# Kernel optimization log

Hardware: AMD Instinct MI355X
Metric: run time of the kernel (lower is better)

## Reference

```python
import jax, jax.numpy as jnp
import numpy as np

N_QUBITS = 8
DIM = 2 ** N_QUBITS  # 256
N_CYCLES = 4
BATCH = 8192

# ---- gate matrices (work for scalar or batched [B] angles) ----

def _rz(t):
    e0 = jnp.exp(-0.5j * t.astype(jnp.complex64))
    e1 = jnp.exp(0.5j * t.astype(jnp.complex64))
    z = jnp.zeros_like(e0)
    return jnp.stack([jnp.stack([e0, z], -1), jnp.stack([z, e1], -1)], -2)


def _ry(t):
    c = jnp.cos(t / 2)
    s = jnp.sin(t / 2)
    m = jnp.stack([jnp.stack([c, -s], -1), jnp.stack([s, c], -1)], -2)
    return m.astype(jnp.complex64)


def _u3(t, p, l):
    ct = jnp.cos(t / 2).astype(jnp.complex64)
    st = jnp.sin(t / 2).astype(jnp.complex64)
    ep = jnp.exp(1j * p.astype(jnp.complex64))
    el = jnp.exp(1j * l.astype(jnp.complex64))
    return jnp.stack([jnp.stack([ct, -el * st], -1),
                      jnp.stack([ep * st, ep * el * ct], -1)], -2)

# ---- state-vector gate application (wire 0 = most significant, torchquantum convention) ----

def apply_1q(psi, U, w):
    B = psi.shape[0]
    p = psi.reshape(B, 2 ** w, 2, -1)
    if U.ndim == 3:
        p = jnp.einsum('bij,bajc->baic', U, p)
    else:
        p = jnp.einsum('ij,bajc->baic', U, p)
    return p.reshape(B, DIM)


def apply_cnot(psi, c, t):
    p = psi.reshape((-1,) + (2,) * N_QUBITS)
    c_ax, t_ax = c + 1, t + 1
    p0 = jax.lax.index_in_dim(p, 0, c_ax, keepdims=True)
    p1 = jnp.flip(jax.lax.index_in_dim(p, 1, c_ax, keepdims=True), axis=t_ax)
    return jnp.concatenate([p0, p1], axis=c_ax).reshape(-1, DIM)


def expval_z(psi, w):
    pr = (psi.real ** 2 + psi.imag ** 2).reshape(psi.shape[0], 2 ** w, 2, -1)
    pr = pr.sum(axis=(1, 3))
    return pr[:, 0] - pr[:, 1]


def conv_block(psi, hi, lo, rza, rzb, rzc, rya, ryb):
    # rz(hi); cnot(hi,lo); rz(lo); ry(hi); cnot(lo,hi); ry(hi); cnot(hi,lo); rz(lo)
    psi = apply_1q(psi, _rz(rza), hi)
    psi = apply_cnot(psi, hi, lo)
    psi = apply_1q(psi, _rz(rzb), lo)
    psi = apply_1q(psi, _ry(rya), hi)
    psi = apply_cnot(psi, lo, hi)
    psi = apply_1q(psi, _ry(ryb), hi)
    psi = apply_cnot(psi, hi, lo)
    psi = apply_1q(psi, _rz(rzc), lo)
    return psi


def _forward(theta, phi, rz_angles, ry_angles, u3_params, w1, b1, w2, b2):
    B = theta.shape[0]
    psi = jnp.zeros((B, DIM), jnp.complex64).at[:, 0].set(1.0)
    # circuit builder (assumed): per cycle RY(theta), RZ(phi) on every wire + CNOT ring
    Ury = _ry(theta)  # [B,2,2]
    Urz = _rz(phi)
    for _ in range(N_CYCLES):
        for w in range(N_QUBITS):
            psi = apply_1q(psi, Ury, w)
        for w in range(N_QUBITS):
            psi = apply_1q(psi, Urz, w)
        for w in range(N_QUBITS):
            psi = apply_cnot(psi, w, (w + 1) % N_QUBITS)
    # conv layer 1: pairs (1,0),(3,2),(5,4),(7,6) using rz1-12, ry1-8
    for i, (hi, lo) in enumerate([(1, 0), (3, 2), (5, 4), (7, 6)]):
        psi = conv_block(psi, hi, lo, rz_angles[3 * i], rz_angles[3 * i + 1],
                         rz_angles[3 * i + 2], ry_angles[2 * i], ry_angles[2 * i + 1])
    # intermediate expvals on [0,2,4,6] are computed-and-discarded in the original (non-collapsing): no-op
    for j, w in enumerate([1, 3, 5, 7]):
        psi = apply_1q(psi, _u3(u3_params[j, 0], u3_params[j, 1], u3_params[j, 2]), w)
    # conv layer 2: pairs (3,1),(7,5),(5,3) using rz13-21, ry9-14
    for k, (hi, lo) in enumerate([(3, 1), (7, 5), (5, 3)]):
        i = 4 + k
        psi = conv_block(psi, hi, lo, rz_angles[3 * i], rz_angles[3 * i + 1],
                         rz_angles[3 * i + 2], ry_angles[2 * i], ry_angles[2 * i + 1])
    # discarded expvals on [1,5]: no-op
    psi = apply_1q(psi, _u3(u3_params[4, 0], u3_params[4, 1], u3_params[4, 2]), 3)
    psi = apply_1q(psi, _u3(u3_params[5, 0], u3_params[5, 1], u3_params[5, 2]), 7)
    x = jnp.stack([expval_z(psi, 3), expval_z(psi, 7)], axis=-1)  # [B,2] real
    h = jnp.tanh(x @ w1.T + b1)
    y = h @ w2.T + b2
    return jax.nn.sigmoid(y)  # [B,1]


def setup_inputs() -> dict:
    key = jax.random.key(0)
    ks = jax.random.split(key, 9)
    return {
        'theta': jax.random.normal(ks[0], (BATCH,), jnp.float32),
        'phi': jax.random.normal(ks[1], (BATCH,), jnp.float32),
        'rz_angles': jax.random.normal(ks[2], (21,), jnp.float32),
        'ry_angles': jax.random.normal(ks[3], (14,), jnp.float32),
        'u3_params': jax.random.normal(ks[4], (6, 3), jnp.float32),
        'w1': jax.random.normal(ks[5], (10, 2), jnp.float32) * 0.5,
        'b1': jax.random.normal(ks[6], (10,), jnp.float32) * 0.1,
        'w2': jax.random.normal(ks[7], (1, 10), jnp.float32) * 0.3,
        'b2': jax.random.normal(ks[8], (1,), jnp.float32) * 0.1,
    }


def reference(theta, phi, rz_angles, ry_angles, u3_params, w1, b1, w2, b2):
    return _forward(theta, phi, rz_angles, ry_angles, u3_params, w1, b1, w2, b2)
```

## Files before the change

kernel.cpp:

```cpp
#include <hip/hip_runtime.h>
#include <math.h>


constexpr int NREG = 8;

typedef float v2f __attribute__((ext_vector_type(2)));

__device__ __forceinline__ v2f vfma(v2f a, v2f b, v2f c) {
  return __builtin_elementwise_fma(a, b, c);
}
__device__ __forceinline__ v2f splat(float x) { return (v2f){x, x}; }

template<int MASK>
__device__ __forceinline__ float lxor(float x) {
  int xi = __float_as_int(x);
  int r;
  if constexpr (MASK == 1)      r = __builtin_amdgcn_mov_dpp(xi, 0xB1, 0xF, 0xF, true);
  else if constexpr (MASK == 2) r = __builtin_amdgcn_mov_dpp(xi, 0x4E, 0xF, 0xF, true);
  else                          r = __builtin_amdgcn_ds_swizzle(xi, (MASK << 10) | 0x1F);
  return __int_as_float(r);
}

template<int MASK>
__device__ __forceinline__ v2f lxor2(v2f v) {
  v2f r;
  r.x = lxor<MASK>(v.x);
  r.y = lxor<MASK>(v.y);
  return r;
}

struct State {
  v2f a[NREG];
};


template<int P>
__device__ __forceinline__ void ry_gate(State& st, float c, float s, int L) {
  if constexpr (P <= 2) {
    constexpr int m = 1 << P;
    #pragma unroll
    for (int r0 = 0; r0 < NREG; ++r0) {
      if (r0 & m) continue;
      const int r1 = r0 | m;
      v2f a0 = st.a[r0], a1 = st.a[r1];
      st.a[r0] = vfma(splat(-s), a1, splat(c) * a0);
      st.a[r1] = vfma(splat( s), a0, splat(c) * a1);
    }
  } else {
    constexpr int m = 1 << (P - 3);
    float ss = ((L >> (P - 3)) & 1) ? s : -s;
    #pragma unroll
    for (int r = 0; r < NREG; ++r) {
      v2f b = lxor2<m>(st.a[r]);
      st.a[r] = vfma(splat(ss), b, splat(c) * st.a[r]);
    }
  }
}

template<int P>
__device__ __forceinline__ void rz_gate(State& st, float cz, float sz, int L) {
  if constexpr (P <= 2) {
    #pragma unroll
    for (int r = 0; r < NREG; ++r) {
      float sg = ((r >> P) & 1) ? sz : -sz;
      v2f v = st.a[r];
      st.a[r] = vfma((v2f){-sg, sg}, v.yx, splat(cz) * v);
    }
  } else {
    float sg = ((L >> (P - 3)) & 1) ? sz : -sz;
    #pragma unroll
    for (int r = 0; r < NREG; ++r) {
      v2f v = st.a[r];
      st.a[r] = vfma((v2f){-sg, sg}, v.yx, splat(cz) * v);
    }
  }
}

template<int PC, int PT>
__device__ __forceinline__ void cnot_gate(State& st, int L) {
  if constexpr (PT <= 2) {
    constexpr int mt = 1 << PT;
    if constexpr (PC <= 2) {
      constexpr int mc = 1 << PC;
      #pragma unroll
      for (int r0 = 0; r0 < NREG; ++r0) {
        if (!(r0 & mc) || (r0 & mt)) continue;
        const int r1 = r0 | mt;
        v2f t = st.a[r0]; st.a[r0] = st.a[r1]; st.a[r1] = t;
      }
    } else {
      bool cb = (L >> (PC - 3)) & 1;
      #pragma unroll
      for (int r0 = 0; r0 < NREG; ++r0) {
        if (r0 & mt) continue;
        const int r1 = r0 | mt;
        v2f a0 = st.a[r0], a1 = st.a[r1];
        st.a[r0] = cb ? a1 : a0;
        st.a[r1] = cb ? a0 : a1;
      }
    }
  } else {
    constexpr int mt = 1 << (PT - 3);
    if constexpr (PC <= 2) {
      constexpr int mc = 1 << PC;
      #pragma unroll
      for (int r = 0; r < NREG; ++r) {
        if (!(r & mc)) continue;
        st.a[r] = lxor2<mt>(st.a[r]);
      }
    } else {
      bool cb = (L >> (PC - 3)) & 1;
      #pragma unroll
      for (int r = 0; r < NREG; ++r) {
        v2f b = lxor2<mt>(st.a[r]);
        st.a[r] = cb ? b : st.a[r];
      }
    }
  }
}

__device__ __forceinline__ v2f cmac(v2f t, v2f u, v2f v) {
  t = vfma(splat(u.x), v, t);
  t = vfma((v2f){-u.y, u.y}, v.yx, t);
  return t;
}

__device__ __forceinline__ v2f ld2(const float* p) {
  return (v2f){p[0], p[1]};
}


template<int MH, int ML>
__device__ __forceinline__ void apply_G_ll(State& st, const float* g, int L) {
  const int bh = (L & MH) ? 1 : 0;
  const int bl = (L & ML) ? 1 : 0;
  const int row = (bh << 1) | bl;
  const float* gr = g + row * 8;
  const v2f cS = ld2(gr + 2 * row);
  const v2f cL = ld2(gr + 2 * (row ^ 1));
  const v2f cH = ld2(gr + 2 * (row ^ 2));
  const v2f cB = ld2(gr + 2 * (row ^ 3));
  #pragma unroll
  for (int r = 0; r < NREG; ++r) {
    v2f v = st.a[r];
    v2f pl = lxor2<ML>(v);
    v2f ph = lxor2<MH>(v);
    v2f pb = lxor2<MH | ML>(v);
    v2f t = (v2f){0.f, 0.f};
    t = cmac(t, cS, v);
    t = cmac(t, cL, pl);
    t = cmac(t, cH, ph);
    t = cmac(t, cB, pb);
    st.a[r] = t;
  }
}

template<int MHR, int MLR>
__device__ __forceinline__ void apply_G_rr(State& st, const float* g) {
  #pragma unroll
  for (int base = 0; base < NREG; ++base) {
    if (base & (MHR | MLR)) continue;
    v2f in0 = st.a[base];
    v2f in1 = st.a[base | MLR];
    v2f in2 = st.a[base | MHR];
    v2f in3 = st.a[base | MHR | MLR];
    #pragma unroll
    for (int i = 0; i < 4; ++i) {
      v2f t = (v2f){0.f, 0.f};
      t = cmac(t, ld2(g + i * 8 + 0), in0);
      t = cmac(t, ld2(g + i * 8 + 2), in1);
      t = cmac(t, ld2(g + i * 8 + 4), in2);
      t = cmac(t, ld2(g + i * 8 + 6), in3);
      if (i == 0) st.a[base] = t;
      else if (i == 1) st.a[base | MLR] = t;
      else if (i == 2) st.a[base | MHR] = t;
      else st.a[base | MHR | MLR] = t;
    }
  }
}

template<int MREG, int ML>
__device__ __forceinline__ void apply_G_mx(State& st, const float* g, int L) {
  const int bl = (L & ML) ? 1 : 0;
  const int r0w = bl;
  const int r1w = 2 + bl;
  const float* g0 = g + r0w * 8;
  const float* g1 = g + r1w * 8;
  const v2f c0S = ld2(g0 + 2 * r0w),       c0L = ld2(g0 + 2 * (r0w ^ 1));
  const v2f c0H = ld2(g0 + 2 * (r0w ^ 2)), c0B = ld2(g0 + 2 * (r0w ^ 3));
  const v2f c1S = ld2(g1 + 2 * r1w),       c1L = ld2(g1 + 2 * (r1w ^ 1));
  const v2f c1H = ld2(g1 + 2 * (r1w ^ 2)), c1B = ld2(g1 + 2 * (r1w ^ 3));
  v2f x[NREG];
  #pragma unroll
  for (int r = 0; r < NREG; ++r) x[r] = lxor2<ML>(st.a[r]);
  v2f o[NREG];
  #pragma unroll
  for (int r = 0; r < NREG; ++r) {
    v2f t = (v2f){0.f, 0.f};
    if (r & MREG) {
      t = cmac(t, c1S, st.a[r]);
      t = cmac(t, c1L, x[r]);
      t = cmac(t, c1H, st.a[r ^ MREG]);
      t = cmac(t, c1B, x[r ^ MREG]);
    } else {
      t = cmac(t, c0S, st.a[r]);
      t = cmac(t, c0L, x[r]);
      t = cmac(t, c0H, st.a[r ^ MREG]);
      t = cmac(t, c0B, x[r ^ MREG]);
    }
    o[r] = t;
  }
  #pragma unroll
  for (int r = 0; r < NREG; ++r) st.a[r] = o[r];
}


__device__ __forceinline__ void b_phase(float* cr, float* ci, int i, float pc, float ps) {
  float r = cr[i] * pc - ci[i] * ps;
  float m = cr[i] * ps + ci[i] * pc;
  cr[i] = r; ci[i] = m;
}
__device__ __forceinline__ void b_rz_hi(float* cr, float* ci, float t) {
  float s, c; sincosf(0.5f * t, &s, &c);
  b_phase(cr, ci, 0, c, -s); b_phase(cr, ci, 1, c, -s);
  b_phase(cr, ci, 2, c,  s); b_phase(cr, ci, 3, c,  s);
}
__device__ __forceinline__ void b_rz_lo(float* cr, float* ci, float t) {
  float s, c; sincosf(0.5f * t, &s, &c);
  b_phase(cr, ci, 0, c, -s); b_phase(cr, ci, 2, c, -s);
  b_phase(cr, ci, 1, c,  s); b_phase(cr, ci, 3, c,  s);
}
__device__ __forceinline__ void b_ry_hi(float* cr, float* ci, float t) {
  float s, c; sincosf(0.5f * t, &s, &c);
  #pragma unroll
  for (int lo = 0; lo < 2; ++lo) {
    int i0 = lo, i1 = 2 + lo;
    float n0r = c * cr[i0] - s * cr[i1], n0i = c * ci[i0] - s * ci[i1];
    float n1r = s * cr[i0] + c * cr[i1], n1i = s * ci[i0] + c * ci[i1];
    cr[i0] = n0r; ci[i0] = n0i; cr[i1] = n1r; ci[i1] = n1i;
  }
}
__device__ __forceinline__ void b_swap(float* cr, float* ci, int i, int j) {
  float t;
  t = cr[i]; cr[i] = cr[j]; cr[j] = t;
  t = ci[i]; ci[i] = ci[j]; ci[j] = t;
}
__device__ __forceinline__ void b_u2(float* cr, float* ci, int i0, int i1,
    float u00r, float u00i, float u01r, float u01i,
    float u10r, float u10i, float u11r, float u11i) {
  float v0r = cr[i0], v0i = ci[i0], v1r = cr[i1], v1i = ci[i1];
  cr[i0] = u00r*v0r - u00i*v0i + u01r*v1r - u01i*v1i;
  ci[i0] = u00r*v0i + u00i*v0r + u01r*v1i + u01i*v1r;
  cr[i1] = u10r*v0r - u10i*v0i + u11r*v1r - u11i*v1i;
  ci[i1] = u10r*v0i + u10i*v0r + u11r*v1i + u11i*v1r;
}
__device__ __forceinline__ void b_u3(float* cr, float* ci, bool on_hi,
                                     float t, float p, float l) {
  float st_, ct, sp, cp, sl, cl;
  sincosf(0.5f * t, &st_, &ct);
  sincosf(p, &sp, &cp);
  sincosf(l, &sl, &cl);
  float u00r = ct,        u00i = 0.f;
  float u01r = -cl * st_, u01i = -sl * st_;
  float u10r = cp * st_,  u10i = sp * st_;
  float eplr = cp * cl - sp * sl, epli = sp * cl + cp * sl;
  float u11r = eplr * ct, u11i = epli * ct;
  if (on_hi) {
    b_u2(cr, ci, 0, 2, u00r,u00i,u01r,u01i,u10r,u10i,u11r,u11i);
    b_u2(cr, ci, 1, 3, u00r,u00i,u01r,u01i,u10r,u10i,u11r,u11i);
  } else {
    b_u2(cr, ci, 0, 1, u00r,u00i,u01r,u01i,u10r,u10i,u11r,u11i);
    b_u2(cr, ci, 2, 3, u00r,u00i,u01r,u01i,u10r,u10i,u11r,u11i);
  }
}


__global__ __launch_bounds__(64, 1) void build_gates_kernel(
    const float* __restrict__ rz_a, const float* __restrict__ ry_a,
    const float* __restrict__ u3_p, float* __restrict__ ws) {
  const int tid = threadIdx.x;
  if (tid >= 28) return;
  const int t = tid >> 2;
  const int j = tid & 3;
  float cr[4] = {0.f, 0.f, 0.f, 0.f};
  float ci[4] = {0.f, 0.f, 0.f, 0.f};
  cr[j] = 1.f;
  b_rz_hi(cr, ci, rz_a[3 * t]);
  b_swap(cr, ci, 2, 3);
  b_rz_lo(cr, ci, rz_a[3 * t + 1]);
  b_ry_hi(cr, ci, ry_a[2 * t]);
  b_swap(cr, ci, 1, 3);
  b_ry_hi(cr, ci, ry_a[2 * t + 1]);
  b_swap(cr, ci, 2, 3);
  b_rz_lo(cr, ci, rz_a[3 * t + 2]);
  if (t < 4)       b_u3(cr, ci, true,  u3_p[3*t], u3_p[3*t+1], u3_p[3*t+2]);
  else if (t == 5) b_u3(cr, ci, true,  u3_p[15],  u3_p[16],    u3_p[17]);
  else if (t == 6) b_u3(cr, ci, false, u3_p[12],  u3_p[13],    u3_p[14]);
  #pragma unroll
  for (int i = 0; i < 4; ++i) {
    ws[t * 32 + i * 8 + j * 2]     = cr[i];
    ws[t * 32 + i * 8 + j * 2 + 1] = ci[i];
  }
}


__global__ __launch_bounds__(256, 4) void qcnn_kernel(
    const float* __restrict__ theta, const float* __restrict__ phi,
    const float* __restrict__ ws,
    const float* __restrict__ w1, const float* __restrict__ b1,
    const float* __restrict__ w2, const float* __restrict__ b2,
    float* __restrict__ out, int B) {
  __shared__ float sG[7 * 32] __attribute__((aligned(16)));
  __shared__ float s_w1[20];
  __shared__ float s_b1[10];
  __shared__ float s_w2[10];
  __shared__ float s_b2[1];

  const int tid = threadIdx.x;
  if (tid < 224) sG[tid] = ws[tid];
  if (tid < 20) s_w1[tid] = w1[tid];
  else if (tid >= 32 && tid < 42) s_b1[tid - 32] = b1[tid - 32];
  else if (tid >= 64 && tid < 74) s_w2[tid - 64] = w2[tid - 64];
  else if (tid == 96) s_b2[0] = b2[0];
  __syncthreads();

  const int L = tid & 31;
  const int g = (blockIdx.x * blockDim.x + tid) >> 5;
  if (g < B) {
    float th = theta[g], ph = phi[g];
    float cth, sth; sincosf(0.5f * th, &sth, &cth);
    float cph, sph; sincosf(0.5f * ph, &sph, &cph);

    State st;
    #pragma unroll
    for (int r = 0; r < NREG; ++r) st.a[r] = (v2f){0.f, 0.f};
    st.a[0].x = (L == 0) ? 1.f : 0.f;

    #pragma unroll 1
    for (int cyc = 0; cyc < 4; ++cyc) {
      ry_gate<7>(st, cth, sth, L);
      ry_gate<6>(st, cth, sth, L);
      ry_gate<5>(st, cth, sth, L);
      ry_gate<4>(st, cth, sth, L);
      ry_gate<3>(st, cth, sth, L);
      ry_gate<2>(st, cth, sth, L);
      ry_gate<1>(st, cth, sth, L);
      ry_gate<0>(st, cth, sth, L);
      rz_gate<7>(st, cph, sph, L);
      rz_gate<6>(st, cph, sph, L);
      rz_gate<5>(st, cph, sph, L);
      rz_gate<4>(st, cph, sph, L);
      rz_gate<3>(st, cph, sph, L);
      rz_gate<2>(st, cph, sph, L);
      rz_gate<1>(st, cph, sph, L);
      rz_gate<0>(st, cph, sph, L);
      cnot_gate<7,6>(st, L);
      cnot_gate<6,5>(st, L);
      cnot_gate<5,4>(st, L);
      cnot_gate<4,3>(st, L);
      cnot_gate<3,2>(st, L);
      cnot_gate<2,1>(st, L);
      cnot_gate<1,0>(st, L);
      cnot_gate<0,7>(st, L);
    }

    apply_G_ll<8, 16>(st, sG + 0 * 32, L);
    apply_G_ll<2, 4>(st, sG + 1 * 32, L);
    apply_G_mx<4, 1>(st, sG + 2 * 32, L);
    apply_G_rr<1, 2>(st, sG + 3 * 32);
    apply_G_ll<2, 8>(st, sG + 4 * 32, L);
    apply_G_rr<1, 4>(st, sG + 5 * 32);
    apply_G_mx<4, 2>(st, sG + 6 * 32, L);

    float s3 = 0.f, s7 = 0.f;
    #pragma unroll
    for (int r = 0; r < NREG; ++r) {
      v2f sq = st.a[r] * st.a[r];
      float p = sq.x + sq.y;
      s3 += p;
      s7 += (r & 1) ? -p : p;
    }
    if ((L >> 1) & 1) s3 = -s3;
    s3 += lxor<1>(s3);  s7 += lxor<1>(s7);
    s3 += lxor<2>(s3);  s7 += lxor<2>(s7);
    s3 += lxor<4>(s3);  s7 += lxor<4>(s7);
    s3 += lxor<8>(s3);  s7 += lxor<8>(s7);
    s3 += lxor<16>(s3); s7 += lxor<16>(s7);

    float y = s_b2[0];
    #pragma unroll
    for (int j = 0; j < 10; ++j) {
      float h = tanhf(fmaf(s3, s_w1[2*j], fmaf(s7, s_w1[2*j+1], s_b1[j])));
      y = fmaf(h, s_w2[j], y);
    }
    float res = 1.f / (1.f + expf(-y));
    if (L == 0) out[g] = res;
  }
}

extern "C" void kernel_launch(void* const* d_in, const int* in_sizes, int n_in,
                              void* d_out, int out_size, void* d_ws, size_t ws_size,
                              hipStream_t stream) {
  const float* theta = (const float*)d_in[0];
  const float* phi   = (const float*)d_in[1];
  const float* rz_a  = (const float*)d_in[2];
  const float* ry_a  = (const float*)d_in[3];
  const float* u3_p  = (const float*)d_in[4];
  const float* w1    = (const float*)d_in[5];
  const float* b1    = (const float*)d_in[6];
  const float* w2    = (const float*)d_in[7];
  const float* b2    = (const float*)d_in[8];
  float* out = (float*)d_out;
  float* ws  = (float*)d_ws;
  const int B = in_sizes[0];

  hipLaunchKernelGGL(build_gates_kernel, dim3(1), dim3(64), 0, stream,
                     rz_a, ry_a, u3_p, ws);

  const int threads = 256;
  const int blocks = (B * 32 + threads - 1) / threads;
  hipLaunchKernelGGL(qcnn_kernel, dim3(blocks), dim3(threads), 0, stream,
                     theta, phi, ws, w1, b1, w2, b2, out, B);
}
```

Measured before the change: 32.08 us.

## Peel first cycle analytically and fuse lane-bit CNOT cascade into one bpermute

The first circuit cycle now starts from |0>, so the layer of RY gates is replaced by a closed-form product state built from cos/sin factors per lane and register. After that come the RZ gates, and the loop runs three times instead of four. The four CNOTs acting on lane-index bits (7..4) are merged into a single ds_bpermute gather using a precomputed prefix-XOR lane permutation. This cuts the number of cross-lane shuffles and the arithmetic of the first cycle. The cost is a dependence on the initial state being |0> and on the bpermute mapping matching the sequential CNOT semantics.

```diff
diff --git a/kernel.cpp b/kernel.cpp
--- a/kernel.cpp
+++ b/kernel.cpp
@@ -119,6 +119,16 @@
   }
 }
 
+__device__ __forceinline__ void cnot_cascade(State& st, int bp_addr) {
+  #pragma unroll
+  for (int r = 0; r < NREG; ++r) {
+    int xr = __builtin_amdgcn_ds_bpermute(bp_addr, __float_as_int(st.a[r].x));
+    int xi = __builtin_amdgcn_ds_bpermute(bp_addr, __float_as_int(st.a[r].y));
+    st.a[r].x = __int_as_float(xr);
+    st.a[r].y = __int_as_float(xi);
+  }
+}
+
 __device__ __forceinline__ v2f cmac(v2f t, v2f u, v2f v) {
   t = vfma(splat(u.x), v, t);
   t = vfma((v2f){-u.y, u.y}, v.yx, t);
@@ -325,6 +335,8 @@
   __syncthreads();
 
   const int L = tid & 31;
+  const int wv = tid & 63;
+  const int bp_addr = ((wv & 32) | ((wv & 31) ^ (((wv & 31) >> 1) & 15))) << 2;
   const int g = (blockIdx.x * blockDim.x + tid) >> 5;
   if (g < B) {
     float th = theta[g], ph = phi[g];
@@ -332,12 +344,34 @@
     float cph, sph; sincosf(0.5f * ph, &sph, &cph);
 
     State st;
-    #pragma unroll
-    for (int r = 0; r < NREG; ++r) st.a[r] = (v2f){0.f, 0.f};
-    st.a[0].x = (L == 0) ? 1.f : 0.f;
+    {
+      float F = (L & 1)  ? sth : cth;
+      F *=      (L & 2)  ? sth : cth;
+      F *=      (L & 4)  ? sth : cth;
+      F *=      (L & 8)  ? sth : cth;
+      F *=      (L & 16) ? sth : cth;
+      #pragma unroll
+      for (int r = 0; r < NREG; ++r) {
+        float X = ((r & 1) ? sth : cth) * ((r & 2) ? sth : cth) * ((r & 4) ? sth : cth);
+        st.a[r] = (v2f){F * X, 0.f};
+      }
+    }
+    rz_gate<7>(st, cph, sph, L);
+    rz_gate<6>(st, cph, sph, L);
+    rz_gate<5>(st, cph, sph, L);
+    rz_gate<4>(st, cph, sph, L);
+    rz_gate<3>(st, cph, sph, L);
+    rz_gate<2>(st, cph, sph, L);
+    rz_gate<1>(st, cph, sph, L);
+    rz_gate<0>(st, cph, sph, L);
+    cnot_cascade(st, bp_addr);
+    cnot_gate<3,2>(st, L);
+    cnot_gate<2,1>(st, L);
+    cnot_gate<1,0>(st, L);
+    cnot_gate<0,7>(st, L);
 
     #pragma unroll 1
-    for (int cyc = 0; cyc < 4; ++cyc) {
+    for (int cyc = 0; cyc < 3; ++cyc) {
       ry_gate<7>(st, cth, sth, L);
       ry_gate<6>(st, cth, sth, L);
       ry_gate<5>(st, cth, sth, L);
@@ -354,10 +388,7 @@
       rz_gate<2>(st, cph, sph, L);
       rz_gate<1>(st, cph, sph, L);
       rz_gate<0>(st, cph, sph, L);
-      cnot_gate<7,6>(st, L);
-      cnot_gate<6,5>(st, L);
-      cnot_gate<5,4>(st, L);
-      cnot_gate<4,3>(st, L);
+      cnot_cascade(st, bp_addr);
       cnot_gate<3,2>(st, L);
       cnot_gate<2,1>(st, L);
       cnot_gate<1,0>(st, L);
```

After: 29.10 us. 9.3% less time.
